# Kernel optimization log

Measured on AMD Instinct MI355X. Metric: run time of the kernel, lower is better.

The kernel has to match this reference:

```python
import jax, jax.numpy as jnp
import numpy as np
import math

D_MODEL = 1024
N_HEAD = 16
HEAD_DIM = D_MODEL // N_HEAD
D_FF = 4096
NUM_STEPS = 100.0
RESCALE = 4000.0
EPS = 1e-5


def _sin_emb(t):
    # SinusoidalPosEmb: t scaled by rescale_steps/num_steps
    half = D_MODEL // 2
    x = t.astype(jnp.float32) / NUM_STEPS * RESCALE
    freqs = jnp.exp(jnp.arange(half, dtype=jnp.float32) * (-math.log(10000.0) / (half - 1)))
    e = x[:, None] * freqs[None, :]
    return jnp.concatenate([jnp.sin(e), jnp.cos(e)], axis=-1)


def _ln(x):
    m = jnp.mean(x, axis=-1, keepdims=True)
    v = jnp.var(x, axis=-1, keepdims=True)
    return (x - m) / jnp.sqrt(v + EPS)


def _gelu2(x):
    return x * jax.nn.sigmoid(1.702 * x)


def setup_inputs() -> dict:
    key = jax.random.key(0)
    ks = jax.random.split(key, 24)
    B, S, D, F = 4, 512, D_MODEL, D_FF
    std = 0.02
    inp = {
        'src': jax.random.normal(ks[0], (B, S, D), dtype=jnp.float32),
        'src_mask': jax.random.randint(ks[1], (B, 1, S, S), 0, 2).astype(bool),
        'timestep': jax.random.randint(ks[2], (B,), 0, 100, dtype=jnp.int32),
        'attention_bias': jax.random.normal(ks[3], (B, N_HEAD, S, S), dtype=jnp.float32),
        # AdaLayerNorm linear: D -> 2D (scale, shift)
        'W_ada': jax.random.normal(ks[4], (D, 2 * D), dtype=jnp.float32) * std,
        'b_ada': jnp.zeros((2 * D,), dtype=jnp.float32),
        'Wq': jax.random.normal(ks[5], (D, D), dtype=jnp.float32) * std,
        'bq': jnp.zeros((D,), dtype=jnp.float32),
        'Wk': jax.random.normal(ks[6], (D, D), dtype=jnp.float32) * std,
        'bk': jnp.zeros((D,), dtype=jnp.float32),
        'Wv': jax.random.normal(ks[7], (D, D), dtype=jnp.float32) * std,
        'bv': jnp.zeros((D,), dtype=jnp.float32),
        'Wo': jax.random.normal(ks[8], (D, D), dtype=jnp.float32) * std,
        'bo': jnp.zeros((D,), dtype=jnp.float32),
        'W1': jax.random.normal(ks[9], (D, F), dtype=jnp.float32) * std,
        'b1': jnp.zeros((F,), dtype=jnp.float32),
        'W2': jax.random.normal(ks[10], (F, D), dtype=jnp.float32) * std,
        'b2': jnp.zeros((D,), dtype=jnp.float32),
        'g2': jnp.ones((D,), dtype=jnp.float32),
        'beta2': jnp.zeros((D,), dtype=jnp.float32),
    }
    return inp


def reference(src, src_mask, timestep, attention_bias, W_ada, b_ada,
              Wq, bq, Wk, bk, Wv, bv, Wo, bo, W1, b1, W2, b2, g2, beta2):
    B, S, D = src.shape
    # AdaLayerNorm: LN(x) * (1 + scale) + shift, scale/shift from timestep emb
    emb = jax.nn.silu(_sin_emb(timestep)) @ W_ada + b_ada  # [B, 2D]
    scale, shift = jnp.split(emb[:, None, :], 2, axis=-1)  # each [B,1,D]
    x = _ln(src) * (1.0 + scale) + shift

    # Self-attention with spatial bias + fp32 masked softmax
    q = (x @ Wq + bq).reshape(B, S, N_HEAD, HEAD_DIM).transpose(0, 2, 1, 3)
    k = (x @ Wk + bk).reshape(B, S, N_HEAD, HEAD_DIM).transpose(0, 2, 1, 3)
    v = (x @ Wv + bv).reshape(B, S, N_HEAD, HEAD_DIM).transpose(0, 2, 1, 3)
    scores = jnp.einsum('bhqd,bhkd->bhqk', q / math.sqrt(HEAD_DIM), k)
    scores = scores + attention_bias
    scores = jnp.where(src_mask, -jnp.inf, scores.astype(jnp.float32))
    probs = jax.nn.softmax(scores, axis=-1).astype(v.dtype)
    ctx = jnp.einsum('bhqk,bhkd->bhqd', probs, v)
    ctx = ctx.transpose(0, 2, 1, 3).reshape(B, S, D)
    x = x + (ctx @ Wo + bo)  # residual from AdaLN output (as in source)

    # FFN with gelu2 on LN2(x)
    h = _ln(x) * g2 + beta2
    ff = _gelu2(h @ W1 + b1) @ W2 + b2
    return x + ff
```

## Files before the change

kernel.cpp:

```cpp
#include <hip/hip_runtime.h>
#include <math.h>

typedef __bf16 bf16x8 __attribute__((ext_vector_type(8)));
typedef float  f32x4  __attribute__((ext_vector_type(4)));
typedef unsigned short u16x8 __attribute__((ext_vector_type(8)));

__device__ __forceinline__ float bf2f(unsigned short u) {
    return __uint_as_float(((unsigned int)u) << 16);
}
__device__ __forceinline__ unsigned short f2bf_n(float f) {
    return __builtin_bit_cast(unsigned short, (__bf16)f);
}
__device__ __forceinline__ void gl_lds16(const unsigned short* g, unsigned short* l) {
    __builtin_amdgcn_global_load_lds(
        (const __attribute__((address_space(1))) unsigned int*)g,
        (__attribute__((address_space(3))) unsigned int*)l, 16, 0, 0);
}

#define BATCH 4
#define SEQ 512
#define DM 1024
#define NH 16
#define DH 64
#define DFF 4096
#define MROWS (BATCH * SEQ)

__global__ __launch_bounds__(256) void fill0_kernel(float* __restrict__ out) {
    out[blockIdx.x * 256 + threadIdx.x] = 0.0f;
}

__global__ __launch_bounds__(256) void tconv_kernel(const float* __restrict__ in,
                                                    unsigned short* __restrict__ out,
                                                    int K, int N) {
    __shared__ float tile[64][33];
    const int n0 = blockIdx.x * 32, k0 = blockIdx.y * 64;
    const int t = threadIdx.x;
    const int tx = t & 31, ty = t >> 5;
    #pragma unroll
    for (int i = 0; i < 8; ++i)
        tile[ty + i * 8][tx] = in[(size_t)(k0 + ty + i * 8) * N + n0 + tx];
    __syncthreads();
    const int nr = t >> 3;
    const int ks = (t & 7) * 8;
    u16x8 v;
    #pragma unroll
    for (int j = 0; j < 8; ++j) v[j] = f2bf_n(tile[ks + j][nr]);
    *(u16x8*)&out[(size_t)(n0 + nr) * K + k0 + ks] = v;
}

__global__ __launch_bounds__(256) void tconv4_kernel(const float* __restrict__ i0,
                                                     const float* __restrict__ i1,
                                                     const float* __restrict__ i2,
                                                     const float* __restrict__ i3,
                                                     unsigned short* __restrict__ o0,
                                                     unsigned short* __restrict__ o1,
                                                     unsigned short* __restrict__ o2,
                                                     unsigned short* __restrict__ o3) {
    const int z = blockIdx.z;
    const float* in = (z == 0) ? i0 : (z == 1) ? i1 : (z == 2) ? i2 : i3;
    unsigned short* out = (z == 0) ? o0 : (z == 1) ? o1 : (z == 2) ? o2 : o3;
    __shared__ float tile[64][33];
    const int n0 = blockIdx.x * 32, k0 = blockIdx.y * 64;
    const int t = threadIdx.x;
    const int tx = t & 31, ty = t >> 5;
    #pragma unroll
    for (int i = 0; i < 8; ++i)
        tile[ty + i * 8][tx] = in[(size_t)(k0 + ty + i * 8) * 1024 + n0 + tx];
    __syncthreads();
    const int nr = t >> 3;
    const int ks = (t & 7) * 8;
    u16x8 v;
    #pragma unroll
    for (int j = 0; j < 8; ++j) v[j] = f2bf_n(tile[ks + j][nr]);
    *(u16x8*)&out[(size_t)(n0 + nr) * 1024 + k0 + ks] = v;
}

__global__ void semb_kernel(const int* __restrict__ ts, float* __restrict__ semb) {
    int b = blockIdx.x;
    float x = (float)ts[b] * 40.0f;
    for (int j = threadIdx.x; j < 1024; j += 256) {
        int idx = (j < 512) ? j : (j - 512);
        float fr = expf(-9.210340371976184f * (float)idx / 511.0f);
        float e = x * fr;
        float v = (j < 512) ? sinf(e) : cosf(e);
        semb[b * 1024 + j] = v / (1.0f + expf(-v));
    }
}

__global__ __launch_bounds__(256) void ada_part_kernel(const float* __restrict__ semb,
                                                       const float* __restrict__ W,
                                                       float* __restrict__ part) {
    const int nb = blockIdx.x, kc = blockIdx.y;
    const int t = threadIdx.x;
    __shared__ float e_s[4][64];
    e_s[t >> 6][t & 63] = semb[(t >> 6) * 1024 + kc * 64 + (t & 63)];
    __syncthreads();
    const int n = nb * 128 + (t & 127);
    const int half = t >> 7;
    float a0 = 0.f, a1 = 0.f, a2 = 0.f, a3 = 0.f;
    const int kk0 = half * 32;
    #pragma unroll 8
    for (int kk = kk0; kk < kk0 + 32; ++kk) {
        const float w = W[(size_t)(kc * 64 + kk) * 2048 + n];
        a0 += e_s[0][kk] * w; a1 += e_s[1][kk] * w;
        a2 += e_s[2][kk] * w; a3 += e_s[3][kk] * w;
    }
    const int j = kc * 2 + half;
    float* p = part + (size_t)j * 4 * 2048 + n;
    p[0] = a0; p[2048] = a1; p[2 * 2048] = a2; p[3 * 2048] = a3;
}

__global__ __launch_bounds__(256) void ada_red_kernel(const float* __restrict__ part,
                                                      const float* __restrict__ bias,
                                                      float* __restrict__ ss) {
    const int idx = blockIdx.x * 256 + threadIdx.x;
    const int b = idx >> 11, n = idx & 2047;
    float acc = bias[n];
    #pragma unroll 8
    for (int j = 0; j < 32; ++j) acc += part[((size_t)j * 4 + b) * 2048 + n];
    ss[b * 2048 + n] = acc;
}

__global__ __launch_bounds__(256) void adaln_kernel(const float* __restrict__ src,
                                                    const float* __restrict__ ss,
                                                    unsigned short* __restrict__ xb) {
    int r = blockIdx.x;
    int b = r >> 9;
    int t = threadIdx.x;
    float4 v4 = *reinterpret_cast<const float4*>(&src[(size_t)r * DM + t * 4]);
    float v[4] = {v4.x, v4.y, v4.z, v4.w};
    float s = v[0] + v[1] + v[2] + v[3];
    float q = v[0]*v[0] + v[1]*v[1] + v[2]*v[2] + v[3]*v[3];
    #pragma unroll
    for (int off = 32; off > 0; off >>= 1) { s += __shfl_down(s, off); q += __shfl_down(q, off); }
    __shared__ float red[8];
    if ((t & 63) == 0) { red[t >> 6] = s; red[4 + (t >> 6)] = q; }
    __syncthreads();
    s = red[0] + red[1] + red[2] + red[3];
    q = red[4] + red[5] + red[6] + red[7];
    float mean = s * (1.0f / DM);
    float var = q * (1.0f / DM) - mean * mean;
    float rstd = rsqrtf(var + 1e-5f);
    ushort4 o;
    o.x = f2bf_n((v[0]-mean)*rstd*(1.0f+ss[b*2048 + t*4+0]) + ss[b*2048+1024 + t*4+0]);
    o.y = f2bf_n((v[1]-mean)*rstd*(1.0f+ss[b*2048 + t*4+1]) + ss[b*2048+1024 + t*4+1]);
    o.z = f2bf_n((v[2]-mean)*rstd*(1.0f+ss[b*2048 + t*4+2]) + ss[b*2048+1024 + t*4+2]);
    o.w = f2bf_n((v[3]-mean)*rstd*(1.0f+ss[b*2048 + t*4+3]) + ss[b*2048+1024 + t*4+3]);
    *reinterpret_cast<ushort4*>(&xb[(size_t)r * DM + t * 4]) = o;
}

__global__ __launch_bounds__(256) void ln2_kernel(const unsigned short* __restrict__ x,
                                                  const float* __restrict__ g2,
                                                  const float* __restrict__ beta2,
                                                  unsigned short* __restrict__ hout) {
    int r = blockIdx.x;
    int t = threadIdx.x;
    ushort4 s4 = *reinterpret_cast<const ushort4*>(&x[(size_t)r * DM + t * 4]);
    float v[4] = {bf2f(s4.x), bf2f(s4.y), bf2f(s4.z), bf2f(s4.w)};
    float s = v[0] + v[1] + v[2] + v[3];
    float q = v[0]*v[0] + v[1]*v[1] + v[2]*v[2] + v[3]*v[3];
    #pragma unroll
    for (int off = 32; off > 0; off >>= 1) { s += __shfl_down(s, off); q += __shfl_down(q, off); }
    __shared__ float red[8];
    if ((t & 63) == 0) { red[t >> 6] = s; red[4 + (t >> 6)] = q; }
    __syncthreads();
    s = red[0] + red[1] + red[2] + red[3];
    q = red[4] + red[5] + red[6] + red[7];
    float mean = s * (1.0f / DM);
    float var = q * (1.0f / DM) - mean * mean;
    float rstd = rsqrtf(var + 1e-5f);
    ushort4 o;
    o.x = f2bf_n((v[0]-mean)*rstd*g2[t*4+0] + beta2[t*4+0]);
    o.y = f2bf_n((v[1]-mean)*rstd*g2[t*4+1] + beta2[t*4+1]);
    o.z = f2bf_n((v[2]-mean)*rstd*g2[t*4+2] + beta2[t*4+2]);
    o.w = f2bf_n((v[3]-mean)*rstd*g2[t*4+3] + beta2[t*4+3]);
    *reinterpret_cast<ushort4*>(&hout[(size_t)r * DM + t * 4]) = o;
}

__global__ __launch_bounds__(256) void merge4_kernel(const unsigned short* __restrict__ P0,
                                                     const unsigned short* __restrict__ P1,
                                                     const unsigned short* __restrict__ P2,
                                                     const unsigned short* __restrict__ P3,
                                                     const float* __restrict__ b2,
                                                     const unsigned short* __restrict__ x2,
                                                     float* __restrict__ out) {
    const size_t i4 = ((size_t)blockIdx.x * 256 + threadIdx.x) * 4;
    const int c = (int)(i4 & 1023);
    ushort4 p0 = *(const ushort4*)&P0[i4];
    ushort4 p1 = *(const ushort4*)&P1[i4];
    ushort4 p2 = *(const ushort4*)&P2[i4];
    ushort4 p3 = *(const ushort4*)&P3[i4];
    ushort4 xx = *(const ushort4*)&x2[i4];
    float4 bb = *(const float4*)&b2[c];
    float4 o;
    o.x = bf2f(p0.x) + bf2f(p1.x) + bf2f(p2.x) + bf2f(p3.x) + bb.x + bf2f(xx.x);
    o.y = bf2f(p0.y) + bf2f(p1.y) + bf2f(p2.y) + bf2f(p3.y) + bb.y + bf2f(xx.y);
    o.z = bf2f(p0.z) + bf2f(p1.z) + bf2f(p2.z) + bf2f(p3.z) + bb.z + bf2f(xx.z);
    o.w = bf2f(p0.w) + bf2f(p1.w) + bf2f(p2.w) + bf2f(p3.w) + bb.w + bf2f(xx.w);
    *(float4*)&out[i4] = o;
}

template<int MODE, int TN, int SELMODE>
__global__ __launch_bounds__(256) void gemm_gl(
    const unsigned short* __restrict__ A,
    const unsigned short* __restrict__ Wta, const unsigned short* __restrict__ Wtb,
    const unsigned short* __restrict__ Wtc,
    const float* __restrict__ ba, const float* __restrict__ bbb, const float* __restrict__ bc,
    const unsigned short* __restrict__ resid,
    unsigned short* __restrict__ oa, unsigned short* __restrict__ ob,
    unsigned short* __restrict__ oc, unsigned short* __restrict__ od,
    float* __restrict__ outF,
    int M, int N, int K, int lda, int ldk)
{
    constexpr int CR  = 128 + TN;
    constexpr int RPW = CR / 4;
    constexpr int NI  = RPW / 8;
    constexpr int WAVE_N = (TN == 128) ? 2 : 1;
    constexpr int WAVE_M = 4 / WAVE_N;
    constexpr int AM = 128 / (WAVE_M * 16);
    constexpr int AN = TN / (WAVE_N * 16);
    constexpr int BUF = CR * 64;

    __shared__ unsigned short LDSu[2 * BUF];

    const int gx = gridDim.x, gy = gridDim.y;
    const int nwg = gx * gy * gridDim.z;
    const int wid = blockIdx.x + gx * (blockIdx.y + gy * blockIdx.z);
    const int aid = (wid & 7) * (nwg >> 3) + (wid >> 3);
    const int plane = gx * gy;
    const int sel = aid / plane;
    const int pid = aid % plane;
    const int by = pid % gy;
    const int bx = pid / gy;

    const unsigned short* Wt;
    const float* bias;
    unsigned short* outB;
    int koff;
    if (SELMODE == 0) {
        Wt = (sel == 0) ? Wta : (sel == 1) ? Wtb : Wtc;
        bias = (sel == 0) ? ba : (sel == 1) ? bbb : bc;
        outB = (sel == 0) ? oa : (sel == 1) ? ob : oc;
        koff = 0;
    } else {
        Wt = Wta; bias = ba;
        outB = (sel == 0) ? oa : (sel == 1) ? ob : (sel == 2) ? oc : od;
        koff = sel * K;
    }

    const int t = threadIdx.x;
    const int lane = t & 63;
    const int w = t >> 6;
    const int l15 = lane & 15, l4 = lane >> 4;
    const int wm = w / WAVE_N, wn = w % WAVE_N;
    const int m0 = by * 128, n0 = bx * TN;

    f32x4 acc[AM][AN];
    #pragma unroll
    for (int i = 0; i < AM; ++i)
        #pragma unroll
        for (int j = 0; j < AN; ++j)
            #pragma unroll
            for (int r = 0; r < 4; ++r) acc[i][j][r] = 0.0f;

    const int gg = (lane & 7) ^ (lane >> 3);
    const unsigned short* gp[NI];
    unsigned short* lp[NI];
    #pragma unroll
    for (int i = 0; i < NI; ++i) {
        const int cr = w * RPW + i * 8 + (lane >> 3);
        gp[i] = (cr < 128) ? (A + (size_t)(m0 + cr) * lda + koff + gg * 8)
                           : (Wt + (size_t)(n0 + cr - 128) * ldk + koff + gg * 8);
        lp[i] = LDSu + (w * RPW + i * 8) * 64;
    }

    const int NT = K / 64;
    #pragma unroll
    for (int i = 0; i < NI; ++i) gl_lds16(gp[i], lp[i]);
    __syncthreads();

    for (int kt = 0; kt < NT; ++kt) {
        const int cur = kt & 1;
        if (kt + 1 < NT) {
            const int k0 = (kt + 1) * 64;
            const int nxo = (cur ^ 1) * BUF;
            #pragma unroll
            for (int i = 0; i < NI; ++i) gl_lds16(gp[i] + k0, lp[i] + nxo);
        }
        const unsigned short* Lb = LDSu + cur * BUF;
        #pragma unroll
        for (int kk = 0; kk < 2; ++kk) {
            const int slot = ((kk * 4 + l4) ^ (l15 & 7)) * 8;
            bf16x8 af[AM], bfr[AN];
            #pragma unroll
            for (int mt = 0; mt < AM; ++mt) {
                const int row = wm * (AM * 16) + mt * 16 + l15;
                u16x8 tmp = *(const u16x8*)(Lb + row * 64 + slot);
                af[mt] = __builtin_bit_cast(bf16x8, tmp);
            }
            #pragma unroll
            for (int nt = 0; nt < AN; ++nt) {
                const int row = 128 + wn * (AN * 16) + nt * 16 + l15;
                u16x8 tmp = *(const u16x8*)(Lb + row * 64 + slot);
                bfr[nt] = __builtin_bit_cast(bf16x8, tmp);
            }
            #pragma unroll
            for (int mt = 0; mt < AM; ++mt)
                #pragma unroll
                for (int nt = 0; nt < AN; ++nt)
                    acc[mt][nt] = __builtin_amdgcn_mfma_f32_16x16x32_bf16(
                        af[mt], bfr[nt], acc[mt][nt], 0, 0, 0);
        }
        if (kt + 1 < NT) __syncthreads();
    }

    #pragma unroll
    for (int mt = 0; mt < AM; ++mt) {
        const int mbase = m0 + wm * (AM * 16) + mt * 16 + l4 * 4;
        #pragma unroll
        for (int nt = 0; nt < AN; ++nt) {
            const int n = n0 + wn * (AN * 16) + nt * 16 + l15;
            const float bs = (MODE == 5) ? 0.0f : bias[n];
            #pragma unroll
            for (int r = 0; r < 4; ++r) {
                const int m = mbase + r;
                float v = acc[mt][nt][r] + bs;
                if (MODE == 2) v = v / (1.0f + expf(-1.702f * v));
                if (MODE == 1 || MODE == 3) v += bf2f(resid[(size_t)m * N + n]);
                if (MODE == 3) outF[(size_t)m * N + n] = v;
                else           outB[(size_t)m * N + n] = f2bf_n(v);
            }
        }
    }
}

#define QB2 32
#define AKT 64
#define KROW 72
#define VROW 72
#define PROW 72
#define SBPIT 72

__global__ __launch_bounds__(128) void attn_mfma(const unsigned short* __restrict__ qbuf,
                                                 const unsigned short* __restrict__ kbuf,
                                                 const unsigned short* __restrict__ vbuf,
                                                 const float* __restrict__ attb,
                                                 const int* __restrict__ mask,
                                                 unsigned short* __restrict__ ctx) {
    __shared__ unsigned short Ks[AKT * KROW];
    __shared__ unsigned short Vt[DH * VROW];
    __shared__ unsigned short Pb[2 * 16 * PROW];
    __shared__ unsigned short Sb[QB2 * SBPIT];
    const int t = threadIdx.x;
    const int lane = t & 63;
    const int w = t >> 6;
    const int l15 = lane & 15, l4 = lane >> 4;
    const int q0 = blockIdx.x * QB2;
    const int h = blockIdx.y;
    const int b = blockIdx.z;

    bf16x8 qf[2];
    {
        const unsigned short* qrow = qbuf + ((size_t)(b * SEQ + q0 + w * 16 + l15)) * DM + h * DH;
        u16x8 t0 = *(const u16x8*)(qrow + l4 * 8);
        u16x8 t1 = *(const u16x8*)(qrow + 32 + l4 * 8);
        qf[0] = __builtin_bit_cast(bf16x8, t0);
        qf[1] = __builtin_bit_cast(bf16x8, t1);
    }

    float m[4] = {-1e30f, -1e30f, -1e30f, -1e30f};
    float l[4] = {0.0f, 0.0f, 0.0f, 0.0f};
    f32x4 o[4];
    #pragma unroll
    for (int dt = 0; dt < 4; ++dt)
        #pragma unroll
        for (int r = 0; r < 4; ++r) o[dt][r] = 0.0f;

    unsigned short* Pw = Pb + w * 16 * PROW;

    const int kr = t >> 1, c0 = (t & 1) * 32;
    const int kp = t & 31, vg = t >> 5;

    u16x8 rk0, rk1, rk2, rk3, rv0, rv1, rv2, rv3;
    float4 rb[4];
    int4   rm[4];

#define LOADT(KT) {                                                                     \
    const int kbase = (KT) * AKT;                                                       \
    const unsigned short* gk = kbuf + ((size_t)(b * SEQ + kbase + kr)) * DM + h * DH + c0; \
    rk0 = *(const u16x8*)gk;        rk1 = *(const u16x8*)(gk + 8);                      \
    rk2 = *(const u16x8*)(gk + 16); rk3 = *(const u16x8*)(gk + 24);                     \
    const unsigned short* gv = vbuf + ((size_t)(b * SEQ + kbase + 2 * kp)) * DM + h * DH + vg * 8; \
    rv0 = *(const u16x8*)gv;        rv1 = *(const u16x8*)(gv + DM);                     \
    rv2 = *(const u16x8*)(gv + 32); rv3 = *(const u16x8*)(gv + DM + 32);                \
    const float* bp = attb + (((size_t)(b * NH + h)) * SEQ + (q0 + w * 16)) * SEQ + kbase; \
    const int* mp = mask + ((size_t)(b * SEQ) + q0 + w * 16) * SEQ + kbase;             \
    _Pragma("unroll")                                                                   \
    for (int i = 0; i < 4; ++i) {                                                       \
        const int e = lane + i * 64; const int row = e >> 4, cg = e & 15;               \
        rb[i] = *(const float4*)&bp[(size_t)row * SEQ + cg * 4];                        \
        rm[i] = *(const int4*)&mp[(size_t)row * SEQ + cg * 4];                          \
    } }

#define STORET() {                                                                      \
    unsigned short* s = Ks + kr * KROW + c0;                                            \
    *(u16x8*)s = rk0; *(u16x8*)(s + 8) = rk1;                                           \
    *(u16x8*)(s + 16) = rk2; *(u16x8*)(s + 24) = rk3;                                   \
    unsigned int* vt32 = (unsigned int*)Vt;                                             \
    _Pragma("unroll")                                                                   \
    for (int j = 0; j < 8; ++j) {                                                       \
        vt32[(vg * 8 + j) * (VROW / 2) + kp] =                                          \
            (unsigned int)rv0[j] | ((unsigned int)rv1[j] << 16);                        \
        vt32[((vg + 4) * 8 + j) * (VROW / 2) + kp] =                                    \
            (unsigned int)rv2[j] | ((unsigned int)rv3[j] << 16);                        \
    }                                                                                   \
    _Pragma("unroll")                                                                   \
    for (int i = 0; i < 4; ++i) {                                                       \
        const int e = lane + i * 64; const int row = e >> 4, cg = e & 15;               \
        ushort4 cc;                                                                     \
        cc.x = f2bf_n(rm[i].x ? -8e30f : 8.0f * rb[i].x);                               \
        cc.y = f2bf_n(rm[i].y ? -8e30f : 8.0f * rb[i].y);                               \
        cc.z = f2bf_n(rm[i].z ? -8e30f : 8.0f * rb[i].z);                               \
        cc.w = f2bf_n(rm[i].w ? -8e30f : 8.0f * rb[i].w);                               \
        *(ushort4*)&Sb[(w * 16 + row) * SBPIT + cg * 4] = cc;                           \
    } }

    LOADT(0);
    const int NT = SEQ / AKT;
    for (int kt = 0; kt < NT; ++kt) {
        __syncthreads();
        STORET();
        __syncthreads();
        if (kt + 1 < NT) LOADT(kt + 1);

        f32x4 acc[4];
        #pragma unroll
        for (int nt = 0; nt < 4; ++nt)
            #pragma unroll
            for (int r = 0; r < 4; ++r)
                acc[nt][r] = bf2f(Sb[(w * 16 + l4 * 4 + r) * SBPIT + nt * 16 + l15]);

        __builtin_amdgcn_s_setprio(1);
        #pragma unroll
        for (int kk = 0; kk < 2; ++kk) {
            #pragma unroll
            for (int nt = 0; nt < 4; ++nt) {
                u16x8 tmp = *(const u16x8*)(Ks + (nt * 16 + l15) * KROW + kk * 32 + l4 * 8);
                acc[nt] = __builtin_amdgcn_mfma_f32_16x16x32_bf16(
                    qf[kk], __builtin_bit_cast(bf16x8, tmp), acc[nt], 0, 0, 0);
            }
        }
        __builtin_amdgcn_s_setprio(0);

        float pm[4] = {-1e30f, -1e30f, -1e30f, -1e30f};
        #pragma unroll
        for (int nt = 0; nt < 4; ++nt) {
            #pragma unroll
            for (int r = 0; r < 4; ++r) {
                const float sv = acc[nt][r] * 0.125f;
                acc[nt][r] = sv;
                pm[r] = fmaxf(pm[r], sv);
            }
        }
        #pragma unroll
        for (int r = 0; r < 4; ++r) {
            #pragma unroll
            for (int off = 1; off < 16; off <<= 1)
                pm[r] = fmaxf(pm[r], __shfl_xor(pm[r], off));
        }
        float al[4], ps[4];
        #pragma unroll
        for (int r = 0; r < 4; ++r) {
            const float mn = fmaxf(m[r], pm[r]);
            al[r] = __expf(m[r] - mn);
            m[r] = mn;
            ps[r] = 0.0f;
        }
        #pragma unroll
        for (int nt = 0; nt < 4; ++nt) {
            #pragma unroll
            for (int r = 0; r < 4; ++r) {
                const float p = __expf(acc[nt][r] - m[r]);
                acc[nt][r] = p;
                ps[r] += p;
            }
        }
        #pragma unroll
        for (int r = 0; r < 4; ++r) {
            #pragma unroll
            for (int off = 1; off < 16; off <<= 1) ps[r] += __shfl_xor(ps[r], off);
            l[r] = l[r] * al[r] + ps[r];
        }
        #pragma unroll
        for (int dt = 0; dt < 4; ++dt)
            #pragma unroll
            for (int r = 0; r < 4; ++r) o[dt][r] *= al[r];

        #pragma unroll
        for (int nt = 0; nt < 4; ++nt)
            #pragma unroll
            for (int r = 0; r < 4; ++r)
                Pw[(l4 * 4 + r) * PROW + nt * 16 + l15] = f2bf_n(acc[nt][r]);

        __builtin_amdgcn_s_setprio(1);
        #pragma unroll
        for (int ks = 0; ks < 2; ++ks) {
            u16x8 pa = *(const u16x8*)(Pw + l15 * PROW + ks * 32 + l4 * 8);
            #pragma unroll
            for (int dt = 0; dt < 4; ++dt) {
                u16x8 vv = *(const u16x8*)(Vt + (dt * 16 + l15) * VROW + ks * 32 + l4 * 8);
                o[dt] = __builtin_amdgcn_mfma_f32_16x16x32_bf16(
                    __builtin_bit_cast(bf16x8, pa), __builtin_bit_cast(bf16x8, vv),
                    o[dt], 0, 0, 0);
            }
        }
        __builtin_amdgcn_s_setprio(0);
    }

    #pragma unroll
    for (int r = 0; r < 4; ++r) {
        const float inv = 1.0f / l[r];
        const size_t row = (size_t)(b * SEQ + q0 + w * 16 + l4 * 4 + r) * DM + h * DH;
        #pragma unroll
        for (int dt = 0; dt < 4; ++dt)
            ctx[row + dt * 16 + l15] = f2bf_n(o[dt][r] * inv);
    }
#undef LOADT
#undef STORET
}

extern "C" void kernel_launch(void* const* d_in, const int* in_sizes, int n_in,
                              void* d_out, int out_size, void* d_ws, size_t ws_size,
                              hipStream_t stream) {
    const float* src  = (const float*)d_in[0];
    const int*   mask = (const int*)d_in[1];
    const int*   ts   = (const int*)d_in[2];
    const float* attb = (const float*)d_in[3];
    const float* Wada = (const float*)d_in[4];
    const float* bada = (const float*)d_in[5];
    const float* Wq   = (const float*)d_in[6];
    const float* bq   = (const float*)d_in[7];
    const float* Wk   = (const float*)d_in[8];
    const float* bk   = (const float*)d_in[9];
    const float* Wv   = (const float*)d_in[10];
    const float* bv   = (const float*)d_in[11];
    const float* Wo   = (const float*)d_in[12];
    const float* bo   = (const float*)d_in[13];
    const float* W1   = (const float*)d_in[14];
    const float* b1   = (const float*)d_in[15];
    const float* W2   = (const float*)d_in[16];
    const float* b2   = (const float*)d_in[17];
    const float* g2   = (const float*)d_in[18];
    const float* bt2  = (const float*)d_in[19];
    float* out = (float*)d_out;

    const size_t MB = 1024 * 1024;
    const size_t NEED_FULL = 65536 + 52 * MB;
    if (ws_size < NEED_FULL) {
        fill0_kernel<<<(size_t)MROWS * DM / 256, 256, 0, stream>>>(out);
        return;
    }

    char* ws = (char*)d_ws;
    float* semb = (float*)(ws + 4096);
    float* ss   = (float*)(ws + 24576);
    char*  base = ws + 65536;
    unsigned short* slotA = (unsigned short*)(base);
    unsigned short* slotB = (unsigned short*)(base + 4 * MB);
    unsigned short* slotC = (unsigned short*)(base + 8 * MB);
    unsigned short* vb   = (unsigned short*)d_out;
    unsigned short* ctxb = (unsigned short*)((char*)d_out + 4 * MB);
    unsigned short* xb = slotA;
    unsigned short* qb = slotB;
    unsigned short* kb = slotC;
    unsigned short* x2 = slotB;
    unsigned short* hb = slotC;
    float* adap = (float*)slotC;

    unsigned short* Wtq = (unsigned short*)(base + 12 * MB);
    unsigned short* Wtk = Wtq + 1024 * 1024;
    unsigned short* Wtv = Wtk + 1024 * 1024;
    unsigned short* Wto = Wtv + 1024 * 1024;
    unsigned short* Wt1 = Wto + 1024 * 1024;
    unsigned short* Wt2 = Wt1 + (size_t)4096 * 1024;
    unsigned short* midF = (unsigned short*)(base + 36 * MB);
    unsigned short* P0 = slotA;
    unsigned short* P1 = slotC;
    unsigned short* P2 = Wtq;
    unsigned short* P3 = Wtv;

    tconv4_kernel<<<dim3(32, 16, 4), 256, 0, stream>>>(Wq, Wk, Wv, Wo, Wtq, Wtk, Wtv, Wto);
    tconv_kernel<<<dim3(128, 16), 256, 0, stream>>>(W1, Wt1, 1024, 4096);
    tconv_kernel<<<dim3(32, 64), 256, 0, stream>>>(W2, Wt2, 4096, 1024);

    semb_kernel<<<4, 256, 0, stream>>>(ts, semb);
    ada_part_kernel<<<dim3(16, 16), 256, 0, stream>>>(semb, Wada, adap);
    ada_red_kernel<<<32, 256, 0, stream>>>(adap, bada, ss);
    adaln_kernel<<<MROWS, 256, 0, stream>>>(src, ss, xb);

    gemm_gl<0, 128, 0><<<dim3(8, 16, 3), 256, 0, stream>>>(
        xb, Wtq, Wtk, Wtv, bq, bk, bv, nullptr, qb, kb, vb, nullptr, nullptr,
        MROWS, DM, DM, DM, DM);
    attn_mfma<<<dim3(SEQ / QB2, NH, BATCH), 128, 0, stream>>>(qb, kb, vb, attb, mask, ctxb);
    gemm_gl<1, 64, 0><<<dim3(16, 16), 256, 0, stream>>>(
        ctxb, Wto, Wto, Wto, bo, bo, bo, xb, x2, x2, x2, nullptr, nullptr,
        MROWS, DM, DM, DM, DM);
    ln2_kernel<<<MROWS, 256, 0, stream>>>(x2, g2, bt2, hb);
    gemm_gl<2, 128, 0><<<dim3(32, 16), 256, 0, stream>>>(
        hb, Wt1, Wt1, Wt1, b1, b1, b1, nullptr, midF, midF, midF, nullptr, nullptr,
        MROWS, DFF, DM, DM, DM);
    gemm_gl<5, 128, 1><<<dim3(8, 16, 4), 256, 0, stream>>>(
        midF, Wt2, Wt2, Wt2, b2, b2, b2, nullptr, P0, P1, P2, P3, nullptr,
        MROWS, DM, 1024, DFF, DFF);
    merge4_kernel<<<(size_t)MROWS * DM / 1024, 256, 0, stream>>>(P0, P1, P2, P3, b2, x2, out);
}
```

Baseline: 159.4 us.

## Add dedicated 4-stage pipelined GEMM for FFN1 with XCD-aware block remap

Replaces the generic gemm_gl launch for the first FFN matmul (with gelu2 epilogue) with a specialized kernel. The new kernel stages A and W tiles straight into LDS through global_load_lds with a 4-deep ring buffer and explicit vmcnt waits, and uses an XOR swizzle on the LDS layout. It also remaps workgroup IDs so that neighbouring tiles land on the same XCD. The goal is to hide global load latency and improve L2 reuse, at the cost of more LDS per block (64KB), which may lower occupancy. Hand-placed waitcnt and barriers add a risk of subtle sync errors.

```diff
diff --git a/kernel.cpp b/kernel.cpp
--- a/kernel.cpp
+++ b/kernel.cpp
@@ -198,6 +198,106 @@
     o.z = bf2f(p0.z) + bf2f(p1.z) + bf2f(p2.z) + bf2f(p3.z) + bb.z + bf2f(xx.z);
     o.w = bf2f(p0.w) + bf2f(p1.w) + bf2f(p2.w) + bf2f(p3.w) + bb.w + bf2f(xx.w);
     *(float4*)&out[i4] = o;
+}
+
+__global__ __launch_bounds__(256) void gemm_cv(
+    const unsigned short* __restrict__ A,
+    const unsigned short* __restrict__ Wt,
+    const float* __restrict__ bias,
+    unsigned short* __restrict__ outB,
+    int N, int lda, int ldk)
+{
+    constexpr int NT = 32;
+    constexpr int BUFU = 256 * 32;
+    __shared__ unsigned short LDSu[4 * BUFU];
+
+    const int gx = gridDim.x, gy = gridDim.y;
+    const int nwg = gx * gy;
+    const int wid = blockIdx.x + gx * blockIdx.y;
+    const int aid = (wid & 7) * (nwg >> 3) + (wid >> 3);
+    const int by = aid % gy;
+    const int bx = aid / gy;
+
+    const int t = threadIdx.x;
+    const int lane = t & 63;
+    const int w = t >> 6;
+    const int l15 = lane & 15, l4 = lane >> 4;
+    const int wm = w >> 1, wn = w & 1;
+    const int m0 = by * 128, n0 = bx * 128;
+
+    float bs[4];
+    #pragma unroll
+    for (int nt = 0; nt < 4; ++nt) bs[nt] = bias[n0 + wn * 64 + nt * 16 + l15];
+
+    f32x4 acc[4][4];
+    #pragma unroll
+    for (int i = 0; i < 4; ++i)
+        #pragma unroll
+        for (int j = 0; j < 4; ++j)
+            #pragma unroll
+            for (int r = 0; r < 4; ++r) acc[i][j][r] = 0.0f;
+
+    const int gg = (lane & 3) ^ ((lane >> 2) & 3) ^ (lane >> 4);
+    const unsigned short* gp[4];
+    unsigned short* lp[4];
+    #pragma unroll
+    for (int i = 0; i < 4; ++i) {
+        const int cr = w * 64 + i * 16 + (lane >> 2);
+        gp[i] = (cr < 128) ? (A + (size_t)(m0 + cr) * lda + gg * 8)
+                           : (Wt + (size_t)(n0 + cr - 128) * ldk + gg * 8);
+        lp[i] = LDSu + (w * 64 + i * 16) * 32;
+    }
+    const int sl = (l4 ^ (l15 & 3) ^ ((l15 >> 2) & 3)) * 8;
+
+#define STG(KT) { const int k0s = (KT) * 32; const int bo = ((KT) & 3) * BUFU;          \
+    _Pragma("unroll") for (int i = 0; i < 4; ++i) gl_lds16(gp[i] + k0s, lp[i] + bo); }
+
+#define CMP(KT) { const unsigned short* Lb = LDSu + ((KT) & 3) * BUFU;                  \
+    bf16x8 af[4], bfr[4];                                                               \
+    _Pragma("unroll") for (int mt = 0; mt < 4; ++mt) {                                  \
+        u16x8 tmp = *(const u16x8*)(Lb + (wm * 64 + mt * 16 + l15) * 32 + sl);          \
+        af[mt] = __builtin_bit_cast(bf16x8, tmp); }                                     \
+    _Pragma("unroll") for (int nt = 0; nt < 4; ++nt) {                                  \
+        u16x8 tmp = *(const u16x8*)(Lb + (128 + wn * 64 + nt * 16 + l15) * 32 + sl);    \
+        bfr[nt] = __builtin_bit_cast(bf16x8, tmp); }                                    \
+    _Pragma("unroll") for (int mt = 0; mt < 4; ++mt)                                    \
+        _Pragma("unroll") for (int nt = 0; nt < 4; ++nt)                                \
+            acc[mt][nt] = __builtin_amdgcn_mfma_f32_16x16x32_bf16(                      \
+                af[mt], bfr[nt], acc[mt][nt], 0, 0, 0); }
+
+    STG(0); STG(1); STG(2);
+    for (int kt = 0; kt < NT - 2; ++kt) {
+        asm volatile("s_waitcnt vmcnt(8)" ::: "memory");
+        __builtin_amdgcn_s_barrier();
+        __builtin_amdgcn_sched_barrier(0);
+        CMP(kt);
+        if (kt + 3 < NT) STG(kt + 3);
+    }
+    asm volatile("s_waitcnt vmcnt(4)" ::: "memory");
+    __builtin_amdgcn_s_barrier();
+    __builtin_amdgcn_sched_barrier(0);
+    CMP(NT - 2);
+    asm volatile("s_waitcnt vmcnt(0)" ::: "memory");
+    __builtin_amdgcn_s_barrier();
+    __builtin_amdgcn_sched_barrier(0);
+    CMP(NT - 1);
+
+    #pragma unroll
+    for (int mt = 0; mt < 4; ++mt) {
+        const int mbase = m0 + wm * 64 + mt * 16 + l4 * 4;
+        #pragma unroll
+        for (int nt = 0; nt < 4; ++nt) {
+            const int n = n0 + wn * 64 + nt * 16 + l15;
+            #pragma unroll
+            for (int r = 0; r < 4; ++r) {
+                float v = acc[mt][nt][r] + bs[nt];
+                v = v / (1.0f + expf(-1.702f * v));
+                outB[(size_t)(mbase + r) * N + n] = f2bf_n(v);
+            }
+        }
+    }
+#undef STG
+#undef CMP
 }
 
 template<int MODE, int TN, int SELMODE>
@@ -606,9 +706,7 @@
         ctxb, Wto, Wto, Wto, bo, bo, bo, xb, x2, x2, x2, nullptr, nullptr,
         MROWS, DM, DM, DM, DM);
     ln2_kernel<<<MROWS, 256, 0, stream>>>(x2, g2, bt2, hb);
-    gemm_gl<2, 128, 0><<<dim3(32, 16), 256, 0, stream>>>(
-        hb, Wt1, Wt1, Wt1, b1, b1, b1, nullptr, midF, midF, midF, nullptr, nullptr,
-        MROWS, DFF, DM, DM, DM);
+    gemm_cv<<<dim3(32, 16), 256, 0, stream>>>(hb, Wt1, b1, midF, DFF, DM, DM);
     gemm_gl<5, 128, 1><<<dim3(8, 16, 4), 256, 0, stream>>>(
         midF, Wt2, Wt2, Wt2, b2, b2, b2, nullptr, P0, P1, P2, P3, nullptr,
         MROWS, DM, 1024, DFF, DFF);
```

New measurement: 161.8 us. About the same (+1.5%).
